# Kernel optimization log

Hardware: AMD Instinct MI355X
Metric: run time of the kernel (lower is better)

## Reference

```python
import jax, jax.numpy as jnp
import numpy as np
import heapq

V = 10000   # vocab size (number of Huffman leaves)
H = 768     # hidden_size
B = 8       # batch
S = 256     # sen_len


def _build_tree():
    """Replicates make_heap/merge_nodes/make_codes: returns padded path tables.
    path_nodes[v, d] = internal-node index (0..V-2) at step d on v's code path,
    path_bits[v, d]  = branch taken (0=left, 1=right), path_mask = valid steps.
    """
    rng = np.random.default_rng(0)
    freqs = rng.integers(1, 1000, size=V)
    heap = [(int(freqs[i]), i, i) for i in range(V)]  # (freq, tiebreak, node_id)
    heapq.heapify(heap)
    left, right = {}, {}
    nid = V
    uid = V
    while len(heap) > 1:
        fa, _, a = heapq.heappop(heap)
        fb, _, b = heapq.heappop(heap)
        left[nid] = a
        right[nid] = b
        heapq.heappush(heap, (fa + fb, uid, nid))
        nid += 1
        uid += 1
    root = heap[0][2]
    paths = [None] * V
    stack = [(root, [], [])]
    while stack:
        n, pn, pb = stack.pop()
        if n < V:
            paths[n] = (pn, pb)
        else:
            idx = n - V  # internal node index into node_W/node_b
            stack.append((left[n], pn + [idx], pb + [0]))
            stack.append((right[n], pn + [idx], pb + [1]))
    D = max(len(p[0]) for p in paths)
    pn = np.zeros((V, D), np.int32)
    pb = np.zeros((V, D), np.int32)
    pm = np.zeros((V, D), bool)
    for i, (ns, bs) in enumerate(paths):
        L = len(ns)
        pn[i, :L] = ns
        pb[i, :L] = bs
        pm[i, :L] = True
    return pn, pb, pm


def setup_inputs() -> dict:
    key = jax.random.key(0)
    k1, k2, k3, k4 = jax.random.split(key, 4)
    pn, pb, pm = _build_tree()
    bound = float(1.0 / np.sqrt(H))  # torch nn.Linear default init
    return {
        "hidden": jax.random.normal(k1, (B, S, H), jnp.float32),
        "target": jax.random.randint(k2, (B, S), 0, V),
        "node_W": jax.random.uniform(k3, (V - 1, H, 2), jnp.float32, -bound, bound),
        "node_b": jax.random.uniform(k4, (V - 1, 2), jnp.float32, -bound, bound),
        "path_nodes": jnp.asarray(pn),
        "path_bits": jnp.asarray(pb),
        "path_mask": jnp.asarray(pm),
    }


def reference(hidden, target, node_W, node_b, path_nodes, path_bits, path_mask):
    # hidden: [B,S,H] -> [T,H]; target: [B,S] -> [T]
    h = hidden.reshape(-1, hidden.shape[-1])
    t = target.reshape(-1)
    nodes = path_nodes[t]          # [T, D] internal-node ids along each token's path
    bits = path_bits[t]            # [T, D] branch targets
    mask = path_mask[t]            # [T, D] valid-step mask
    Wg = node_W[nodes]             # [T, D, H, 2] gathered per-path linear weights
    bg = node_b[nodes]             # [T, D, 2]
    logits = jnp.einsum('th,tdho->tdo', h, Wg) + bg  # [T, D, 2]
    # Faithful to original: CrossEntropyLoss applied to Softmax OUTPUT (double softmax)
    probs = jax.nn.softmax(logits, axis=-1)
    logp = jax.nn.log_softmax(probs, axis=-1)
    ce = -jnp.take_along_axis(logp, bits[..., None], axis=-1)[..., 0]  # [T, D]
    # Original accumulates per-step CE (each over batch of 1) by summation
    return jnp.sum(jnp.where(mask, ce, jnp.zeros_like(ce)))
```

## Files before the change

### kernel.cpp

```cpp
#include <hip/hip_runtime.h>

#define HID 768
#define NTHREADS 256
#define WPB 4
#define RTHREADS 256

__global__ __launch_bounds__(NTHREADS) void huffman_token_kernel(
    const float* __restrict__ hidden,
    const int*   __restrict__ target,
    const float* __restrict__ node_W,
    const float* __restrict__ node_b,
    const int*   __restrict__ path_nodes,
    const int*   __restrict__ path_bits,
    const void*  __restrict__ path_mask,
    float*       __restrict__ partial,
    int D)
{
    const int t    = blockIdx.x;
    const int wave = threadIdx.x >> 6;
    const int lane = threadIdx.x & 63;

    const bool mask_is_byte = (*(const unsigned int*)path_mask) > 1u;

    const int v = target[t];
    const long pbase = (long)v * D;

    bool  my_m = false;
    int   my_n = 0, my_bit = 0;
    float my_b0 = 0.0f, my_b1 = 0.0f;
    if (lane < D) {
        my_m = mask_is_byte
            ? (((const unsigned char*)path_mask)[pbase + lane] != 0)
            : (((const int*)path_mask)[pbase + lane] != 0);
        if (my_m) {
            my_n   = path_nodes[pbase + lane];
            my_bit = path_bits[pbase + lane];
            const float2 b2 = ((const float2*)node_b)[my_n];
            my_b0 = b2.x; my_b1 = b2.y;
        }
    }
    const int depth = __popcll(__ballot(my_m));

    const float2* __restrict__ h2 = (const float2*)(hidden + (long)t * HID);
    float2 h[6];
    #pragma unroll
    for (int j = 0; j < 6; ++j) h[j] = h2[j * 64 + lane];

    float sum = 0.0f;

    const int S = (depth > wave) ? ((depth - wave + WPB - 1) / WPB) : 0;
    if (S > 0) {
        int d = wave;
        int n = __shfl(my_n, d, 64);

        float4 w[6];
        {
            const float4* __restrict__ w4 =
                (const float4*)(node_W + (long)n * (HID * 2));
            #pragma unroll
            for (int j = 0; j < 6; ++j) w[j] = w4[j * 64 + lane];
        }

        for (int i = 0; i < S; ++i) {
            const int dn = d + WPB;
            float4 wn[6];
            if (i + 1 < S) {
                const int nn = __shfl(my_n, dn, 64);
                const float4* __restrict__ w4n =
                    (const float4*)(node_W + (long)nn * (HID * 2));
                #pragma unroll
                for (int j = 0; j < 6; ++j) wn[j] = w4n[j * 64 + lane];
            }

            float acc0 = 0.0f, acc1 = 0.0f;
            #pragma unroll
            for (int j = 0; j < 6; ++j) {
                acc0 += h[j].x * w[j].x + h[j].y * w[j].z;
                acc1 += h[j].x * w[j].y + h[j].y * w[j].w;
            }
            #pragma unroll
            for (int off = 32; off > 0; off >>= 1) {
                acc0 += __shfl_xor(acc0, off, 64);
                acc1 += __shfl_xor(acc1, off, 64);
            }

            const float b0  = __shfl(my_b0, d, 64);
            const float b1  = __shfl(my_b1, d, 64);
            const int   bit = __shfl(my_bit, d, 64);

            const float l0  = acc0 + b0;
            const float l1  = acc1 + b1;
            const float m   = fmaxf(l0, l1);
            const float e0  = __expf(l0 - m);
            const float e1  = __expf(l1 - m);
            const float s   = e0 + e1;
            const float p0  = e0 / s;
            const float p1  = e1 / s;
            const float lse = __logf(__expf(p0) + __expf(p1));
            const float pb  = bit ? p1 : p0;
            sum += lse - pb;

            d = dn;
            if (i + 1 < S) {
                #pragma unroll
                for (int j = 0; j < 6; ++j) w[j] = wn[j];
            }
        }
    }

    if (lane == 0) partial[t * WPB + wave] = sum;
}

__global__ __launch_bounds__(RTHREADS) void huffman_reduce_kernel(
    const float* __restrict__ partial, float* __restrict__ out, int n4)
{
    const float4* __restrict__ p4 = (const float4*)partial;
    float s = 0.0f;
    for (int i = threadIdx.x; i < n4; i += RTHREADS) {
        const float4 v = p4[i];
        s += (v.x + v.y) + (v.z + v.w);
    }
    #pragma unroll
    for (int off = 32; off > 0; off >>= 1) s += __shfl_xor(s, off, 64);
    __shared__ float ws[RTHREADS / 64];
    if ((threadIdx.x & 63) == 0) ws[threadIdx.x >> 6] = s;
    __syncthreads();
    if (threadIdx.x == 0) {
        float tot = 0.0f;
        #pragma unroll
        for (int w = 0; w < RTHREADS / 64; ++w) tot += ws[w];
        out[0] = tot;
    }
}

extern "C" void kernel_launch(void* const* d_in, const int* in_sizes, int n_in,
                              void* d_out, int out_size, void* d_ws, size_t ws_size,
                              hipStream_t stream) {
    const float* hidden     = (const float*)d_in[0];
    const int*   target     = (const int*)d_in[1];
    const float* node_W     = (const float*)d_in[2];
    const float* node_b     = (const float*)d_in[3];
    const int*   path_nodes = (const int*)d_in[4];
    const int*   path_bits  = (const int*)d_in[5];
    const void*  path_mask  = (const void*)d_in[6];
    float* out = (float*)d_out;
    float* partial = (float*)d_ws;

    const int T   = in_sizes[0] / HID;
    const int Vm1 = in_sizes[3] / 2;
    const int V   = Vm1 + 1;
    const int D   = in_sizes[4] / V;

    const int nslot = T * WPB;

    huffman_token_kernel<<<dim3(T), dim3(NTHREADS), 0, stream>>>(
        hidden, target, node_W, node_b, path_nodes, path_bits, path_mask,
        partial, D);

    huffman_reduce_kernel<<<dim3(1), dim3(RTHREADS), 0, stream>>>(
        partial, out, nslot / 4);
}
```

Measured before the change: 118.5 us.

## Drop weight prefetch, use readlane broadcasts and merged dual reduction, raise occupancy

Result: no change. 116.6 us (-1.6%).

```diff
diff --git a/kernel.cpp b/kernel.cpp
--- a/kernel.cpp
+++ b/kernel.cpp
@@ -5,7 +5,7 @@
 #define WPB 4
 #define RTHREADS 256
 
-__global__ __launch_bounds__(NTHREADS) void huffman_token_kernel(
+__global__ __launch_bounds__(NTHREADS, 8) void huffman_token_kernel(
     const float* __restrict__ hidden,
     const int*   __restrict__ target,
     const float* __restrict__ node_W,
@@ -48,64 +48,47 @@
 
     float sum = 0.0f;
 
-    const int S = (depth > wave) ? ((depth - wave + WPB - 1) / WPB) : 0;
-    if (S > 0) {
-        int d = wave;
-        int n = __shfl(my_n, d, 64);
+    for (int d = wave; d < depth; d += WPB) {
+        const int   n   = __builtin_amdgcn_readlane(my_n, d);
+        const int   bit = __builtin_amdgcn_readlane(my_bit, d);
+        const float b0  = __uint_as_float(
+            __builtin_amdgcn_readlane(__float_as_uint(my_b0), d));
+        const float b1  = __uint_as_float(
+            __builtin_amdgcn_readlane(__float_as_uint(my_b1), d));
 
+        const float4* __restrict__ w4 =
+            (const float4*)(node_W + (long)n * (HID * 2));
         float4 w[6];
-        {
-            const float4* __restrict__ w4 =
-                (const float4*)(node_W + (long)n * (HID * 2));
-            #pragma unroll
-            for (int j = 0; j < 6; ++j) w[j] = w4[j * 64 + lane];
+        #pragma unroll
+        for (int j = 0; j < 6; ++j) w[j] = w4[j * 64 + lane];
+
+        float acc0 = 0.0f, acc1 = 0.0f;
+        #pragma unroll
+        for (int j = 0; j < 6; ++j) {
+            acc0 += h[j].x * w[j].x + h[j].y * w[j].z;
+            acc1 += h[j].x * w[j].y + h[j].y * w[j].w;
         }
 
-        for (int i = 0; i < S; ++i) {
-            const int dn = d + WPB;
-            float4 wn[6];
-            if (i + 1 < S) {
-                const int nn = __shfl(my_n, dn, 64);
-                const float4* __restrict__ w4n =
-                    (const float4*)(node_W + (long)nn * (HID * 2));
-                #pragma unroll
-                for (int j = 0; j < 6; ++j) wn[j] = w4n[j * 64 + lane];
-            }
+        float r     = (lane < 32) ? acc0 : acc1;
+        float other = (lane < 32) ? acc1 : acc0;
+        r += __shfl_xor(other, 32, 64);
+        #pragma unroll
+        for (int off = 16; off > 0; off >>= 1) r += __shfl_xor(r, off, 64);
+        const float ro = __shfl_xor(r, 32, 64);
+        const float A0 = (lane < 32) ? r  : ro;
+        const float A1 = (lane < 32) ? ro : r;
 
-            float acc0 = 0.0f, acc1 = 0.0f;
-            #pragma unroll
-            for (int j = 0; j < 6; ++j) {
-                acc0 += h[j].x * w[j].x + h[j].y * w[j].z;
-                acc1 += h[j].x * w[j].y + h[j].y * w[j].w;
-            }
-            #pragma unroll
-            for (int off = 32; off > 0; off >>= 1) {
-                acc0 += __shfl_xor(acc0, off, 64);
-                acc1 += __shfl_xor(acc1, off, 64);
-            }
-
-            const float b0  = __shfl(my_b0, d, 64);
-            const float b1  = __shfl(my_b1, d, 64);
-            const int   bit = __shfl(my_bit, d, 64);
-
-            const float l0  = acc0 + b0;
-            const float l1  = acc1 + b1;
-            const float m   = fmaxf(l0, l1);
-            const float e0  = __expf(l0 - m);
-            const float e1  = __expf(l1 - m);
-            const float s   = e0 + e1;
-            const float p0  = e0 / s;
-            const float p1  = e1 / s;
-            const float lse = __logf(__expf(p0) + __expf(p1));
-            const float pb  = bit ? p1 : p0;
-            sum += lse - pb;
-
-            d = dn;
-            if (i + 1 < S) {
-                #pragma unroll
-                for (int j = 0; j < 6; ++j) w[j] = wn[j];
-            }
-        }
+        const float l0  = A0 + b0;
+        const float l1  = A1 + b1;
+        const float m   = fmaxf(l0, l1);
+        const float e0  = __expf(l0 - m);
+        const float e1  = __expf(l1 - m);
+        const float s   = e0 + e1;
+        const float p0  = e0 / s;
+        const float p1  = e1 / s;
+        const float lse = __logf(__expf(p0) + __expf(p1));
+        const float pb  = bit ? p1 : p0;
+        sum += lse - pb;
     }
 
     if (lane == 0) partial[t * WPB + wave] = sum;
```
